# Kernel optimization log

Hardware: AMD Instinct MI355X
Metric: run time of the kernel (lower is better)

The kernel has to match this reference:

```python
import jax, jax.numpy as jnp
import numpy as np

B, S, D, E, N, K = 4, 2048, 1024, 2048, 16, 4

def setup_inputs() -> dict:
    key = jax.random.key(0)
    ks = jax.random.split(key, 16)
    w = lambda k, shape, s=0.02: jax.random.normal(k, shape, dtype=jnp.float32) * s
    return {
        "x": jax.random.normal(ks[0], (B, S, D), dtype=jnp.float32),
        "ln_g": jnp.ones((D,), jnp.float32),
        "ln_b": jnp.zeros((D,), jnp.float32),
        "W_in": w(ks[1], (2 * E, D)),
        "b_in": jnp.zeros((2 * E,), jnp.float32),
        "conv_w": w(ks[2], (E, 1, K), 0.1),
        "conv_b": jnp.zeros((E,), jnp.float32),
        "A": w(ks[3], (E, N), 0.1),
        "Bm": w(ks[4], (E, N), 0.1),
        "W_c": w(ks[5], (E, E)),
        "b_c": jnp.zeros((E,), jnp.float32),
        "W_d": w(ks[6], (E, E)),
        "b_d": jnp.zeros((E,), jnp.float32),
        "log_delta": jnp.zeros((E,), jnp.float32),
        "W_out": w(ks[7], (D, E)),
        "b_out": jnp.zeros((D,), jnp.float32),
    }

def _layernorm(x, g, b, eps=1e-5):
    mu = jnp.mean(x, axis=-1, keepdims=True)
    var = jnp.var(x, axis=-1, keepdims=True)
    return (x - mu) * jax.lax.rsqrt(var + eps) * g + b

def _forward(x, ln_g, ln_b, W_in, b_in, conv_w, conv_b, A, Bm, W_c, b_c, W_d, b_d, log_delta, W_out, b_out):
    x_ln = _layernorm(x, ln_g, ln_b)
    x_proj = jnp.einsum("bsd,ed->bse", x_ln, W_in) + b_in  # (B,S,2E)
    xp, gate = jnp.split(x_proj, 2, axis=-1)
    # causal depthwise conv1d (torch pads K-1 both sides then truncates -> left pad only)
    xc = jax.lax.conv_general_dilated(
        xp.transpose(0, 2, 1), conv_w, (1,), [(K - 1, 0)],
        dimension_numbers=("NCH", "OIH", "NCH"), feature_group_count=E)
    xc = (xc + conv_b[None, :, None]).transpose(0, 2, 1)  # (B,S,E)
    xc = jax.nn.silu(xc)
    # selective SSM
    delta = jax.nn.softplus(log_delta)
    A_diag = jnp.exp(-delta)  # (E,)
    u = (jnp.einsum("bse,fe->bsf", xc, W_c) + b_c) * jax.nn.sigmoid(jnp.einsum("bse,fe->bsf", xc, W_d) + b_d)
    def step(h, u_t):
        # h: (B,E,N), u_t: (B,E)
        h = h * A_diag[None, :, None] + u_t[:, :, None] * Bm[None]
        y = jnp.sum(h * A[None], axis=-1)  # (B,E)
        return h, y
    h0 = jnp.zeros((x.shape[0], E, N), x.dtype)
    _, ys = jax.lax.scan(step, h0, u.transpose(1, 0, 2))  # ys: (S,B,E)
    x_ssm = ys.transpose(1, 0, 2)
    x_gated = x_ssm * jax.nn.sigmoid(gate)
    out = jnp.einsum("bse,de->bsd", x_gated, W_out) + b_out
    return out + x

def reference(x, ln_g, ln_b, W_in, b_in, conv_w, conv_b, A, Bm, W_c, b_c, W_d, b_d, log_delta, W_out, b_out):
    return _forward(x, ln_g, ln_b, W_in, b_in, conv_w, conv_b, A, Bm, W_c, b_c, W_d, b_d, log_delta, W_out, b_out)
```

## Files before the change

### kernel.cpp

```cpp
#include <hip/hip_runtime.h>
#include <hip/hip_bf16.h>

typedef __bf16 bf16_t;
typedef unsigned char u8;
typedef float  f32x4  __attribute__((ext_vector_type(4)));
typedef int    i32x4  __attribute__((ext_vector_type(4)));
typedef int    i32x8  __attribute__((ext_vector_type(8)));
typedef __attribute__((address_space(3))) unsigned as3u32;
typedef __attribute__((address_space(1))) unsigned as1u32;

#define Bdim 4
#define Sdim 2048
#define Ddim 1024
#define Edim 2048
#define CH 64
#define CL 32

#define WSCALE 32.0f
#define XPSCALE 32.0f
#define XCSCALE 16.0f
#define CSCALE 16.0f
#define GSCALE 256.0f

__device__ __forceinline__ void gload_lds16(const void* g, void* l) {
  __builtin_amdgcn_global_load_lds((const as1u32*)g, (as3u32*)l, 16, 0, 0);
}
__device__ __forceinline__ float sigmoidf_(float x) {
  return 1.f / (1.f + __expf(-x));
}
__device__ __forceinline__ int pk_fp8x4(float a, float b, float c, float d) {
  int p = __builtin_amdgcn_cvt_pk_fp8_f32(a, b, 0, 0);
  p = __builtin_amdgcn_cvt_pk_fp8_f32(c, d, p, 1);
  return p;
}
template<int K>
__device__ __forceinline__ float dq8(int v) {
  return __builtin_amdgcn_cvt_f32_fp8(v, K);
}
__device__ __forceinline__ u8 q8(float v) {
  return (u8)(__builtin_amdgcn_cvt_pk_fp8_f32(v, v, 0, 0) & 0xff);
}

__global__ __launch_bounds__(256)
void cvt_fp8_3(const float* __restrict__ s0, const float* __restrict__ s1,
               const float* __restrict__ s2, u8* __restrict__ d0,
               u8* __restrict__ d1, u8* __restrict__ d2) {
  const int seg = blockIdx.x >> 12;
  const int i   = ((blockIdx.x & 4095) * 256 + threadIdx.x) * 4;
  const float* s = (seg == 0) ? s0 : (seg == 1) ? s1 : s2;
  u8*          d = (seg == 0) ? d0 : (seg == 1) ? d1 : d2;
  *(int*)(d + i) = pk_fp8x4(s[i] * WSCALE, s[i + 1] * WSCALE,
                            s[i + 2] * WSCALE, s[i + 3] * WSCALE);
}

__global__ __launch_bounds__(256)
void cvt_fp8(const float* __restrict__ s, u8* __restrict__ d, int n, float scale) {
  int i = (blockIdx.x * 256 + threadIdx.x) * 4;
  if (i < n)
    *(int*)(d + i) = pk_fp8x4(s[i] * scale, s[i + 1] * scale,
                              s[i + 2] * scale, s[i + 3] * scale);
}

__global__ __launch_bounds__(256)
void prep_scalars(const float* __restrict__ ld, const float* __restrict__ Am,
                  const float* __restrict__ Bm, float* __restrict__ aexp,
                  float* __restrict__ Ce) {
  int e = blockIdx.x * 256 + threadIdx.x;
  if (e >= Edim) return;
  float d = ld[e];
  float sp = (d > 20.f) ? d : log1pf(expf(d));
  aexp[e] = expf(-sp);
  float s = 0.f;
  #pragma unroll
  for (int n = 0; n < 16; ++n) s += Am[e * 16 + n] * Bm[e * 16 + n];
  Ce[e] = s;
}

__global__ __launch_bounds__(256)
void ln_kernel(const float* __restrict__ x, const float* __restrict__ g,
               const float* __restrict__ b, u8* __restrict__ out) {
  const int row = blockIdx.x;
  const int tid = threadIdx.x;
  const float4 v = ((const float4*)(x + (size_t)row * Ddim))[tid];
  float s  = v.x + v.y + v.z + v.w;
  float ss = v.x * v.x + v.y * v.y + v.z * v.z + v.w * v.w;
  #pragma unroll
  for (int o = 32; o > 0; o >>= 1) { s += __shfl_down(s, o); ss += __shfl_down(ss, o); }
  __shared__ float sh[8];
  const int wv = tid >> 6, lane = tid & 63;
  if (lane == 0) { sh[wv] = s; sh[4 + wv] = ss; }
  __syncthreads();
  s  = sh[0] + sh[1] + sh[2] + sh[3];
  ss = sh[4] + sh[5] + sh[6] + sh[7];
  const float mean = s * (1.f / Ddim);
  const float var  = ss * (1.f / Ddim) - mean * mean;
  const float rstd = rsqrtf(var + 1e-5f);
  const float4 gv = ((const float4*)g)[tid];
  const float4 bv = ((const float4*)b)[tid];
  *(int*)(out + (size_t)row * Ddim + tid * 4) =
      pk_fp8x4((v.x - mean) * rstd * gv.x + bv.x,
               (v.y - mean) * rstd * gv.y + bv.y,
               (v.z - mean) * rstd * gv.z + bv.z,
               (v.w - mean) * rstd * gv.w + bv.w);
}

#define BM 128
#define BN 128

template<int MODE>
__global__ __launch_bounds__(256)
void gemm_mx(const u8* __restrict__ A, const u8* __restrict__ Bw,
             const float* __restrict__ bias, const u8* __restrict__ X,
             const float* __restrict__ R, u8* __restrict__ C8,
             float* __restrict__ Cf, float descale, float oscale,
             int M, int N, int K) {
  __shared__ __align__(16) u8 As[BM * 128];
  __shared__ __align__(16) u8 Bs[BN * 128];

  const int tid  = threadIdx.x;
  const int lane = tid & 63;
  const int wv   = tid >> 6;
  const int m0   = blockIdx.y * BM;
  const int n0   = blockIdx.x * BN;

  const int wr = (wv >> 1) * 64;
  const int wc = (wv & 1) * 64;
  const int tq = lane >> 4;
  const int tr = lane & 15;

  f32x4 acc[4][4] = {};

  size_t srcOff[4];
  int    ldsOff[4];
  #pragma unroll
  for (int g = 0; g < 4; ++g) {
    const int p   = g * 256 + tid;
    const int row = p >> 3;
    const int c   = (p & 7) ^ (row & 7);
    srcOff[g] = (size_t)row * K + c * 16;
    ldsOff[g] = g * 4096 + wv * 1024;
  }
  const size_t aBase = (size_t)m0 * K;
  const size_t bBase = (size_t)n0 * K;
  char* AsB = (char*)As;
  char* BsB = (char*)Bs;

  const int s7 = tr & 7;
  const int p0 = (((tq << 1)) ^ s7) * 16;
  const int p1 = (((tq << 1) | 1) ^ s7) * 16;

  for (int k0 = 0; k0 < K; k0 += 128) {
    __syncthreads();
    #pragma unroll
    for (int g = 0; g < 4; ++g)
      gload_lds16(A + aBase + srcOff[g] + k0, AsB + ldsOff[g]);
    #pragma unroll
    for (int g = 0; g < 4; ++g)
      gload_lds16(Bw + bBase + srcOff[g] + k0, BsB + ldsOff[g]);
    __syncthreads();

    i32x8 aF[4], bF[4];
    #pragma unroll
    for (int i = 0; i < 4; ++i) {
      const int rb = (wr + i * 16 + tr) * 128;
      const i32x4 lo = *(const i32x4*)&As[rb + p0];
      const i32x4 hi = *(const i32x4*)&As[rb + p1];
      aF[i] = __builtin_shufflevector(lo, hi, 0, 1, 2, 3, 4, 5, 6, 7);
    }
    #pragma unroll
    for (int j = 0; j < 4; ++j) {
      const int rb = (wc + j * 16 + tr) * 128;
      const i32x4 lo = *(const i32x4*)&Bs[rb + p0];
      const i32x4 hi = *(const i32x4*)&Bs[rb + p1];
      bF[j] = __builtin_shufflevector(lo, hi, 0, 1, 2, 3, 4, 5, 6, 7);
    }
    #pragma unroll
    for (int i = 0; i < 4; ++i)
      #pragma unroll
      for (int j = 0; j < 4; ++j)
        acc[i][j] = __builtin_amdgcn_mfma_scale_f32_16x16x128_f8f6f4(
            aF[i], bF[j], acc[i][j], 0, 0, 0, 0x7F, 0, 0x7F);
  }

  #pragma unroll
  for (int i = 0; i < 4; ++i) {
    #pragma unroll
    for (int j = 0; j < 4; ++j) {
      const int col = n0 + wc + j * 16 + tr;
      const float bv = bias[col];
      #pragma unroll
      for (int r = 0; r < 4; ++r) {
        const int rowg = m0 + wr + i * 16 + tq * 4 + r;
        const size_t idx = (size_t)rowg * N + col;
        const float v = acc[i][j][r] * descale + bv;
        if (MODE == 1) {
          Cf[idx] = v + R[idx];
        } else if (MODE == 2) {
          const float xv = dq8<0>((int)X[idx]);
          C8[idx] = q8(xv * sigmoidf_(v));
        } else {
          C8[idx] = q8(v * oscale);
        }
      }
    }
  }
}

__global__ __launch_bounds__(256)
void conv_silu(const u8* __restrict__ xpg8, const float* __restrict__ cw,
               const float* __restrict__ cb, u8* __restrict__ xc8) {
  const int e0 = (blockIdx.y * 256 + threadIdx.x) * 4;
  const int b  = blockIdx.x >> 9;
  const int s0 = (blockIdx.x & 511) * 4;
  float w[4][4], bias[4];
  #pragma unroll
  for (int k = 0; k < 4; ++k) {
    const float4 wv = *(const float4*)(cw + (e0 + k) * 4);
    w[k][0] = wv.x; w[k][1] = wv.y; w[k][2] = wv.z; w[k][3] = wv.w;
    bias[k] = cb[e0 + k];
  }
  float f[7][4];
  #pragma unroll
  for (int j = 0; j < 7; ++j) {
    const int s = s0 - 3 + j;
    const int xv = (s >= 0) ? *(const int*)(xpg8 + (size_t)(b * Sdim + s) * (2 * Edim) + e0) : 0;
    f[j][0] = dq8<0>(xv); f[j][1] = dq8<1>(xv);
    f[j][2] = dq8<2>(xv); f[j][3] = dq8<3>(xv);
  }
  #pragma unroll
  for (int t = 0; t < 4; ++t) {
    float y[4];
    #pragma unroll
    for (int k = 0; k < 4; ++k) {
      float a = fmaf(w[k][0], f[t][k],
               fmaf(w[k][1], f[t + 1][k],
               fmaf(w[k][2], f[t + 2][k],
                    w[k][3] * f[t + 3][k])));
      a = a * (1.f / XPSCALE) + bias[k];
      y[k] = a * sigmoidf_(a) * XCSCALE;
    }
    *(int*)(xc8 + (size_t)(b * Sdim + s0 + t) * Edim + e0) =
        pk_fp8x4(y[0], y[1], y[2], y[3]);
  }
}

__global__ __launch_bounds__(256)
void scan_part1(const u8* __restrict__ u8p, const float* __restrict__ aexp,
                float* __restrict__ zloc) {
  const int c  = blockIdx.x;
  const int b  = blockIdx.y >> 1;
  const int e0 = ((blockIdx.y & 1) * 256 + threadIdx.x) * 4;
  const float4 av = *(const float4*)(aexp + e0);
  const u8* up = u8p + ((size_t)(b * Sdim + c * CL)) * Edim + e0;
  float z0 = 0.f, z1 = 0.f, z2 = 0.f, z3 = 0.f;
  #pragma unroll
  for (int t = 0; t < CL; ++t) {
    const int uv = *(const int*)(up + (size_t)t * Edim);
    z0 = fmaf(av.x, z0, dq8<0>(uv));
    z1 = fmaf(av.y, z1, dq8<1>(uv));
    z2 = fmaf(av.z, z2, dq8<2>(uv));
    z3 = fmaf(av.w, z3, dq8<3>(uv));
  }
  float4 zv = {z0, z1, z2, z3};
  *(float4*)(zloc + ((size_t)b * CH + c) * Edim + e0) = zv;
}

__global__ __launch_bounds__(256)
void scan_part2(const float* __restrict__ aexp, float* __restrict__ zloc) {
  const int idx = blockIdx.x * 256 + threadIdx.x;
  const int b = idx >> 11, e = idx & (Edim - 1);
  float a  = aexp[e];
  float aL = a * a;
  aL = aL * aL; aL = aL * aL; aL = aL * aL; aL = aL * aL;
  float* zp = zloc + (size_t)b * CH * Edim + e;
  float pref = 0.f;
  #pragma unroll 4
  for (int c = 0; c < CH; ++c) {
    const float loc = zp[(size_t)c * Edim];
    zp[(size_t)c * Edim] = pref;
    pref = fmaf(aL, pref, loc);
  }
}

__global__ __launch_bounds__(256)
void scan_part3(const u8* __restrict__ u8p, const u8* __restrict__ xpg8,
                const float* __restrict__ aexp, const float* __restrict__ Ce,
                const float* __restrict__ zloc, u8* __restrict__ xg8) {
  const int c  = blockIdx.x;
  const int b  = blockIdx.y >> 1;
  const int e0 = ((blockIdx.y & 1) * 256 + threadIdx.x) * 4;
  const float4 av = *(const float4*)(aexp + e0);
  float4 Cv = *(const float4*)(Ce + e0);
  const float cs = GSCALE / CSCALE;
  Cv.x *= cs; Cv.y *= cs; Cv.z *= cs; Cv.w *= cs;
  float4 zv = *(const float4*)(zloc + ((size_t)b * CH + c) * Edim + e0);
  const u8* up = u8p  + ((size_t)(b * Sdim + c * CL)) * Edim + e0;
  const u8* gp = xpg8 + ((size_t)(b * Sdim + c * CL)) * (2 * Edim) + Edim + e0;
  u8*       op = xg8  + ((size_t)(b * Sdim + c * CL)) * Edim + e0;
  #pragma unroll 4
  for (int t = 0; t < CL; ++t) {
    const int uv = *(const int*)(up + (size_t)t * Edim);
    const int gv = *(const int*)(gp + (size_t)t * (2 * Edim));
    zv.x = fmaf(av.x, zv.x, dq8<0>(uv));
    zv.y = fmaf(av.y, zv.y, dq8<1>(uv));
    zv.z = fmaf(av.z, zv.z, dq8<2>(uv));
    zv.w = fmaf(av.w, zv.w, dq8<3>(uv));
    const float y0 = Cv.x * zv.x * sigmoidf_(dq8<0>(gv) * (1.f / XPSCALE));
    const float y1 = Cv.y * zv.y * sigmoidf_(dq8<1>(gv) * (1.f / XPSCALE));
    const float y2 = Cv.z * zv.z * sigmoidf_(dq8<2>(gv) * (1.f / XPSCALE));
    const float y3 = Cv.w * zv.w * sigmoidf_(dq8<3>(gv) * (1.f / XPSCALE));
    *(int*)(op + (size_t)t * Edim) = pk_fp8x4(y0, y1, y2, y3);
  }
}

extern "C" void kernel_launch(void* const* d_in, const int* in_sizes, int n_in,
                              void* d_out, int out_size, void* d_ws, size_t ws_size,
                              hipStream_t stream) {
  const float* x         = (const float*)d_in[0];
  const float* ln_g      = (const float*)d_in[1];
  const float* ln_b      = (const float*)d_in[2];
  const float* W_in      = (const float*)d_in[3];
  const float* b_in      = (const float*)d_in[4];
  const float* conv_w    = (const float*)d_in[5];
  const float* conv_b    = (const float*)d_in[6];
  const float* Am        = (const float*)d_in[7];
  const float* Bm        = (const float*)d_in[8];
  const float* W_c       = (const float*)d_in[9];
  const float* b_c       = (const float*)d_in[10];
  const float* W_d       = (const float*)d_in[11];
  const float* b_d       = (const float*)d_in[12];
  const float* log_delta = (const float*)d_in[13];
  const float* W_out     = (const float*)d_in[14];
  const float* b_out     = (const float*)d_in[15];
  float* out = (float*)d_out;

  const size_t MiB = 1024 * 1024;
  char* w = (char*)d_ws;
  u8*     wWin8  = (u8*)   (w + 0);
  u8*     wWc8   = (u8*)   (w + 4 * MiB);
  u8*     wWd8   = (u8*)   (w + 8 * MiB);
  u8*     wWout8 = (u8*)   (w + 12 * MiB);
  float*  aexp   = (float*)(w + 15 * MiB);
  float*  Ce     = (float*)(w + 15 * MiB + 16384);
  float*  zloc   = (float*)(w + 15 * MiB + 65536);
  u8*     xln8   = (u8*)   (w + 18 * MiB);
  u8*     xpg8   = (u8*)   (w + 26 * MiB);
  u8*     xc8    = (u8*)   (w + 58 * MiB);
  u8*     c8     = (u8*)   (w + 74 * MiB);
  u8*     u8b    = (u8*)   (w + 90 * MiB);
  u8*     xg8    = (u8*)   (w + 106 * MiB);

  const int M = Bdim * Sdim;
  const float dsIn  = 1.f / WSCALE;
  const float dsCD  = 1.f / (WSCALE * XCSCALE);
  const float dsOut = 1.f / (WSCALE * GSCALE);

  cvt_fp8_3<<<3 * 4096, 256, 0, stream>>>(W_in, W_c, W_d, wWin8, wWc8, wWd8);
  cvt_fp8<<<(Ddim * Edim) / 1024, 256, 0, stream>>>(W_out, wWout8, Ddim * Edim, WSCALE);
  prep_scalars<<<Edim / 256, 256, 0, stream>>>(log_delta, Am, Bm, aexp, Ce);

  ln_kernel<<<M, 256, 0, stream>>>(x, ln_g, ln_b, xln8);

  gemm_mx<3><<<dim3((2 * Edim) / BN, M / BM), 256, 0, stream>>>(
      xln8, wWin8, b_in, nullptr, nullptr, xpg8, nullptr, dsIn, XPSCALE, M, 2 * Edim, Ddim);

  conv_silu<<<dim3(Bdim * (Sdim / 4), Edim / 1024), 256, 0, stream>>>(xpg8, conv_w, conv_b, xc8);

  gemm_mx<3><<<dim3(Edim / BN, M / BM), 256, 0, stream>>>(
      xc8, wWc8, b_c, nullptr, nullptr, c8, nullptr, dsCD, CSCALE, M, Edim, Edim);
  gemm_mx<2><<<dim3(Edim / BN, M / BM), 256, 0, stream>>>(
      xc8, wWd8, b_d, c8, nullptr, u8b, nullptr, dsCD, 1.f, M, Edim, Edim);

  scan_part1<<<dim3(CH, Bdim * 2), 256, 0, stream>>>(u8b, aexp, zloc);
  scan_part2<<<(Bdim * Edim) / 256, 256, 0, stream>>>(aexp, zloc);
  scan_part3<<<dim3(CH, Bdim * 2), 256, 0, stream>>>(u8b, xpg8, aexp, Ce, zloc, xg8);

  gemm_mx<1><<<dim3(Ddim / BN, M / BM), 256, 0, stream>>>(
      xg8, wWout8, b_out, nullptr, x, nullptr, out, dsOut, 1.f, M, Ddim, Edim);

  (void)in_sizes; (void)n_in; (void)out_size; (void)ws_size;
}
```

Before: 376.0 us.

## Add 256x256-tile 512-thread MX-fp8 GEMM for input and SSM projections

Introduces a second fp8 MFMA GEMM kernel with 256x256 block tiles, 8 waves per block and double-buffered LDS, where each wave computes a 128x64 sub-tile in two halves that reuse the loaded B fragments. The input projection and both W_c/W_d GEMMs switch to it, while the output projection keeps the old kernel. The larger tile raises arithmetic intensity and cuts global traffic per FLOP. In exchange it uses more registers and 128KB of LDS per block, and produces far fewer blocks (e.g. 256 for the E×E GEMMs), which can hurt occupancy and wave-quantisation across the CUs.

Result: no change. 380.1 us (+1.1%).

```diff
diff --git a/kernel.cpp b/kernel.cpp
--- a/kernel.cpp
+++ b/kernel.cpp
@@ -196,6 +196,129 @@
         if (MODE == 1) {
           Cf[idx] = v + R[idx];
         } else if (MODE == 2) {
+          const float xv = dq8<0>((int)X[idx]);
+          C8[idx] = q8(xv * sigmoidf_(v));
+        } else {
+          C8[idx] = q8(v * oscale);
+        }
+      }
+    }
+  }
+}
+
+#define BM2 256
+#define BN2 256
+
+template<int MODE>
+__global__ __launch_bounds__(512, 2)
+void gemm_mx2(const u8* __restrict__ A, const u8* __restrict__ Bw,
+              const float* __restrict__ bias, const u8* __restrict__ X,
+              u8* __restrict__ C8, float descale, float oscale,
+              int M, int N, int K) {
+  __shared__ __align__(16) u8 As[2][BM2 * 128];
+  __shared__ __align__(16) u8 Bs[2][BN2 * 128];
+
+  const int tid  = threadIdx.x;
+  const int lane = tid & 63;
+  const int wv   = tid >> 6;
+  const int m0   = blockIdx.y * BM2;
+  const int n0   = blockIdx.x * BN2;
+  const int wr   = (wv >> 2) * 128;
+  const int wc   = (wv & 3) * 64;
+  const int tq   = lane >> 4;
+  const int tr   = lane & 15;
+
+  f32x4 acc[8][4] = {};
+
+  const int    srow    = tid >> 3;
+  const int    scol    = (tid & 7) ^ (srow & 7);
+  const size_t sBase   = (size_t)srow * K + (size_t)scol * 16;
+  const size_t rowStep = (size_t)64 * K;
+  const u8* Ap = A  + (size_t)m0 * K + sBase;
+  const u8* Bp = Bw + (size_t)n0 * K + sBase;
+  const int ldsBase = wv * 1024;
+
+  const int s7 = tr & 7;
+  const int p0 = (((tq << 1)) ^ s7) * 16;
+  const int p1 = (((tq << 1) | 1) ^ s7) * 16;
+
+  const int NK = K >> 7;
+
+  #pragma unroll
+  for (int g = 0; g < 4; ++g)
+    gload_lds16(Ap + g * rowStep, (u8*)As[0] + g * 8192 + ldsBase);
+  #pragma unroll
+  for (int g = 0; g < 4; ++g)
+    gload_lds16(Bp + g * rowStep, (u8*)Bs[0] + g * 8192 + ldsBase);
+  __syncthreads();
+
+  for (int t = 0; t < NK; ++t) {
+    const int cur = t & 1;
+    if (t + 1 < NK) {
+      const u8* An = Ap + (size_t)(t + 1) * 128;
+      const u8* Bn = Bp + (size_t)(t + 1) * 128;
+      #pragma unroll
+      for (int g = 0; g < 4; ++g)
+        gload_lds16(An + g * rowStep, (u8*)As[cur ^ 1] + g * 8192 + ldsBase);
+      #pragma unroll
+      for (int g = 0; g < 4; ++g)
+        gload_lds16(Bn + g * rowStep, (u8*)Bs[cur ^ 1] + g * 8192 + ldsBase);
+    }
+    const u8* Ac = (const u8*)As[cur];
+    const u8* Bc = (const u8*)Bs[cur];
+    i32x8 aF[4], bF[4];
+    #pragma unroll
+    for (int j = 0; j < 4; ++j) {
+      const int rb = (wc + j * 16 + tr) * 128;
+      const i32x4 lo = *(const i32x4*)&Bc[rb + p0];
+      const i32x4 hi = *(const i32x4*)&Bc[rb + p1];
+      bF[j] = __builtin_shufflevector(lo, hi, 0, 1, 2, 3, 4, 5, 6, 7);
+    }
+    #pragma unroll
+    for (int i = 0; i < 4; ++i) {
+      const int rb = (wr + i * 16 + tr) * 128;
+      const i32x4 lo = *(const i32x4*)&Ac[rb + p0];
+      const i32x4 hi = *(const i32x4*)&Ac[rb + p1];
+      aF[i] = __builtin_shufflevector(lo, hi, 0, 1, 2, 3, 4, 5, 6, 7);
+    }
+    __builtin_amdgcn_s_setprio(1);
+    #pragma unroll
+    for (int i = 0; i < 4; ++i)
+      #pragma unroll
+      for (int j = 0; j < 4; ++j)
+        acc[i][j] = __builtin_amdgcn_mfma_scale_f32_16x16x128_f8f6f4(
+            aF[i], bF[j], acc[i][j], 0, 0, 0, 0x7F, 0, 0x7F);
+    __builtin_amdgcn_s_setprio(0);
+    #pragma unroll
+    for (int i = 0; i < 4; ++i) {
+      const int rb = (wr + 64 + i * 16 + tr) * 128;
+      const i32x4 lo = *(const i32x4*)&Ac[rb + p0];
+      const i32x4 hi = *(const i32x4*)&Ac[rb + p1];
+      aF[i] = __builtin_shufflevector(lo, hi, 0, 1, 2, 3, 4, 5, 6, 7);
+    }
+    __builtin_amdgcn_s_setprio(1);
+    #pragma unroll
+    for (int i = 0; i < 4; ++i)
+      #pragma unroll
+      for (int j = 0; j < 4; ++j)
+        acc[4 + i][j] = __builtin_amdgcn_mfma_scale_f32_16x16x128_f8f6f4(
+            aF[i], bF[j], acc[4 + i][j], 0, 0, 0, 0x7F, 0, 0x7F);
+    __builtin_amdgcn_s_setprio(0);
+    __syncthreads();
+  }
+
+  #pragma unroll
+  for (int i = 0; i < 8; ++i) {
+    #pragma unroll
+    for (int j = 0; j < 4; ++j) {
+      const int col = n0 + wc + j * 16 + tr;
+      const float bv = bias[col];
+      #pragma unroll
+      for (int r = 0; r < 4; ++r) {
+        const int rowg = m0 + wr + i * 16 + tq * 4 + r;
+        const size_t idx = (size_t)rowg * N + col;
+        const float v = acc[i][j][r] * descale + bv;
+        if (MODE == 2) {
           const float xv = dq8<0>((int)X[idx]);
           C8[idx] = q8(xv * sigmoidf_(v));
         } else {
@@ -361,15 +484,15 @@
 
   ln_kernel<<<M, 256, 0, stream>>>(x, ln_g, ln_b, xln8);
 
-  gemm_mx<3><<<dim3((2 * Edim) / BN, M / BM), 256, 0, stream>>>(
-      xln8, wWin8, b_in, nullptr, nullptr, xpg8, nullptr, dsIn, XPSCALE, M, 2 * Edim, Ddim);
+  gemm_mx2<3><<<dim3((2 * Edim) / BN2, M / BM2), 512, 0, stream>>>(
+      xln8, wWin8, b_in, nullptr, xpg8, dsIn, XPSCALE, M, 2 * Edim, Ddim);
 
   conv_silu<<<dim3(Bdim * (Sdim / 4), Edim / 1024), 256, 0, stream>>>(xpg8, conv_w, conv_b, xc8);
 
-  gemm_mx<3><<<dim3(Edim / BN, M / BM), 256, 0, stream>>>(
-      xc8, wWc8, b_c, nullptr, nullptr, c8, nullptr, dsCD, CSCALE, M, Edim, Edim);
-  gemm_mx<2><<<dim3(Edim / BN, M / BM), 256, 0, stream>>>(
-      xc8, wWd8, b_d, c8, nullptr, u8b, nullptr, dsCD, 1.f, M, Edim, Edim);
+  gemm_mx2<3><<<dim3(Edim / BN2, M / BM2), 512, 0, stream>>>(
+      xc8, wWc8, b_c, nullptr, c8, dsCD, CSCALE, M, Edim, Edim);
+  gemm_mx2<2><<<dim3(Edim / BN2, M / BM2), 512, 0, stream>>>(
+      xc8, wWd8, b_d, c8, u8b, dsCD, 1.f, M, Edim, Edim);
 
   scan_part1<<<dim3(CH, Bdim * 2), 256, 0, stream>>>(u8b, aexp, zloc);
   scan_part2<<<(Bdim * Edim) / 256, 256, 0, stream>>>(aexp, zloc);
```

## Fuse W_c and W_d GEMMs into one dual-accumulator kernel sharing A tiles

Applied to the files above, without the earlier changes.

Replaces the two separate FP8 GEMMs (W_c producing c8, then W_d with a sigmoid-gated epilogue) with a single kernel that loads each xc8 tile once. It computes both products from the same A fragments into two accumulator sets and writes u = c*sigmoid(d) directly. This removes the c8 intermediate round-trip, the repeated read of xc8 and one launch. The cost is a narrower N tile (64 columns per weight), twice the accumulator registers, and no c8 re-quantization step before the gating, which slightly changes rounding.

After: 363.8 us. 1.03x faster.

```diff
diff --git a/kernel.cpp b/kernel.cpp
--- a/kernel.cpp
+++ b/kernel.cpp
@@ -195,12 +195,111 @@
         const float v = acc[i][j][r] * descale + bv;
         if (MODE == 1) {
           Cf[idx] = v + R[idx];
-        } else if (MODE == 2) {
-          const float xv = dq8<0>((int)X[idx]);
-          C8[idx] = q8(xv * sigmoidf_(v));
         } else {
           C8[idx] = q8(v * oscale);
         }
+      }
+    }
+  }
+}
+
+__global__ __launch_bounds__(256)
+void gemm_cu(const u8* __restrict__ A, const u8* __restrict__ Wc8,
+             const u8* __restrict__ Wd8, const float* __restrict__ bias_c,
+             const float* __restrict__ bias_d, u8* __restrict__ U8,
+             float descale, int M, int N, int K) {
+  __shared__ __align__(16) u8 As[128 * 128];
+  __shared__ __align__(16) u8 Bs[128 * 128];
+
+  const int tid  = threadIdx.x;
+  const int lane = tid & 63;
+  const int wv   = tid >> 6;
+  const int m0   = blockIdx.y * 128;
+  const int n0   = blockIdx.x * 64;
+
+  const int wr = (wv >> 1) * 64;
+  const int wc = (wv & 1) * 32;
+  const int tq = lane >> 4;
+  const int tr = lane & 15;
+
+  f32x4 accC[4][2] = {};
+  f32x4 accD[4][2] = {};
+
+  size_t srcOffA[4], srcOffB[4];
+  const u8* bSrc[4];
+  int ldsOff[4];
+  #pragma unroll
+  for (int g = 0; g < 4; ++g) {
+    const int p   = g * 256 + tid;
+    const int row = p >> 3;
+    const int c   = (p & 7) ^ (row & 7);
+    srcOffA[g] = (size_t)row * K + c * 16;
+    srcOffB[g] = (size_t)(n0 + (row & 63)) * K + c * 16;
+    bSrc[g]    = (g < 2) ? Wc8 : Wd8;
+    ldsOff[g]  = g * 4096 + wv * 1024;
+  }
+  const size_t aBase = (size_t)m0 * K;
+  char* AsB = (char*)As;
+  char* BsB = (char*)Bs;
+
+  const int s7 = tr & 7;
+  const int p0 = (((tq << 1)) ^ s7) * 16;
+  const int p1 = (((tq << 1) | 1) ^ s7) * 16;
+
+  for (int k0 = 0; k0 < K; k0 += 128) {
+    __syncthreads();
+    #pragma unroll
+    for (int g = 0; g < 4; ++g)
+      gload_lds16(A + aBase + srcOffA[g] + k0, AsB + ldsOff[g]);
+    #pragma unroll
+    for (int g = 0; g < 4; ++g)
+      gload_lds16(bSrc[g] + srcOffB[g] + k0, BsB + ldsOff[g]);
+    __syncthreads();
+
+    i32x8 aF[4], bC[2], bD[2];
+    #pragma unroll
+    for (int i = 0; i < 4; ++i) {
+      const int rb = (wr + i * 16 + tr) * 128;
+      const i32x4 lo = *(const i32x4*)&As[rb + p0];
+      const i32x4 hi = *(const i32x4*)&As[rb + p1];
+      aF[i] = __builtin_shufflevector(lo, hi, 0, 1, 2, 3, 4, 5, 6, 7);
+    }
+    #pragma unroll
+    for (int j = 0; j < 2; ++j) {
+      const int rbc = (wc + j * 16 + tr) * 128;
+      const i32x4 loc = *(const i32x4*)&Bs[rbc + p0];
+      const i32x4 hic = *(const i32x4*)&Bs[rbc + p1];
+      bC[j] = __builtin_shufflevector(loc, hic, 0, 1, 2, 3, 4, 5, 6, 7);
+      const int rbd = (64 + wc + j * 16 + tr) * 128;
+      const i32x4 lod = *(const i32x4*)&Bs[rbd + p0];
+      const i32x4 hid = *(const i32x4*)&Bs[rbd + p1];
+      bD[j] = __builtin_shufflevector(lod, hid, 0, 1, 2, 3, 4, 5, 6, 7);
+    }
+    #pragma unroll
+    for (int i = 0; i < 4; ++i)
+      #pragma unroll
+      for (int j = 0; j < 2; ++j) {
+        accC[i][j] = __builtin_amdgcn_mfma_scale_f32_16x16x128_f8f6f4(
+            aF[i], bC[j], accC[i][j], 0, 0, 0, 0x7F, 0, 0x7F);
+        accD[i][j] = __builtin_amdgcn_mfma_scale_f32_16x16x128_f8f6f4(
+            aF[i], bD[j], accD[i][j], 0, 0, 0, 0x7F, 0, 0x7F);
+      }
+  }
+
+  #pragma unroll
+  for (int i = 0; i < 4; ++i) {
+    #pragma unroll
+    for (int j = 0; j < 2; ++j) {
+      const int col = n0 + wc + j * 16 + tr;
+      const float bc = bias_c[col];
+      const float bd = bias_d[col];
+      #pragma unroll
+      for (int r = 0; r < 4; ++r) {
+        const int rowg = m0 + wr + i * 16 + tq * 4 + r;
+        const size_t idx = (size_t)rowg * N + col;
+        const float vc = accC[i][j][r] * descale + bc;
+        const float vd = accD[i][j][r] * descale + bd;
+        U8[idx] = q8(vc * CSCALE * sigmoidf_(vd));
       }
     }
   }
@@ -346,7 +445,6 @@
   u8*     xln8   = (u8*)   (w + 18 * MiB);
   u8*     xpg8   = (u8*)   (w + 26 * MiB);
   u8*     xc8    = (u8*)   (w + 58 * MiB);
-  u8*     c8     = (u8*)   (w + 74 * MiB);
   u8*     u8b    = (u8*)   (w + 90 * MiB);
   u8*     xg8    = (u8*)   (w + 106 * MiB);
 
@@ -366,10 +464,8 @@
 
   conv_silu<<<dim3(Bdim * (Sdim / 4), Edim / 1024), 256, 0, stream>>>(xpg8, conv_w, conv_b, xc8);
 
-  gemm_mx<3><<<dim3(Edim / BN, M / BM), 256, 0, stream>>>(
-      xc8, wWc8, b_c, nullptr, nullptr, c8, nullptr, dsCD, CSCALE, M, Edim, Edim);
-  gemm_mx<2><<<dim3(Edim / BN, M / BM), 256, 0, stream>>>(
-      xc8, wWd8, b_d, c8, nullptr, u8b, nullptr, dsCD, 1.f, M, Edim, Edim);
+  gemm_cu<<<dim3(Edim / 64, M / BM), 256, 0, stream>>>(
+      xc8, wWc8, wWd8, b_c, b_d, u8b, dsCD, M, Edim, Edim);
 
   scan_part1<<<dim3(CH, Bdim * 2), 256, 0, stream>>>(u8b, aexp, zloc);
   scan_part2<<<(Bdim * Edim) / 256, 256, 0, stream>>>(aexp, zloc);
```
